# Kernel tuning notes

Hardware: AMD Instinct MI355X
Metric: run time of the kernel (lower is better)

## Reference

```python
import jax, jax.numpy as jnp
import numpy as np

FACTOR = 27.2114 * 0.529177249  # Hartree*Bohr -> eV*Angstrom coulomb factor
N_TYPES = 6
NEURON = [25, 50, 100]
AXIS = 16
B, NC, NM = 4, 128, 16384


def _dense_stack(x, channels, params):
    """Type-indexed MLP: x (B,N,F), channels (N,) int -> (B,N,neuron[-1]).
    Layer 0: no residual; layers 1,2: out=2*in -> residual via concat([x,x])."""
    res_modes = [0, 2, 2]
    for (W, b), res in zip(params, res_modes):
        # W: (C, out, in); gather per-position weights, contract input features
        y = jnp.tanh(jnp.einsum('bnf,nof->bno', x, W[channels]) + b[channels][None])
        if res == 2:
            y = y + jnp.concatenate([x, x], axis=-1)
        elif res == 1:
            y = y + x
        x = y
    return x


def _fwd(atom_coords, charge_coords, charges, esp_params, ef_params, atom_types, real_mask):
    Bb, Nc, _ = atom_coords.shape
    # ---- local environment (off-diagonal neighbor pairs) ----
    i = jnp.arange(Nc)[:, None]
    j = jnp.arange(Nc - 1)[None, :]
    nidx = jnp.where(j < i, j, j + 1)                              # (Nc, Nc-1) neighbor indices
    rij = atom_coords[:, :, None] - atom_coords[:, None]           # (B,Nc,Nc,3)
    rij_off = jnp.take_along_axis(rij, nidx[None, :, :, None], axis=2)  # (B,Nc,Nc-1,3)
    dij = jnp.linalg.norm(rij_off, axis=-1)                        # (B,Nc,Nc-1)
    loc_env_a = rij_off / (dij * dij)[..., None]                   # rij / r^2

    # ---- masked ESP / E-field from MM charges ----
    rq = atom_coords[:, :, None] - charge_coords[:, None]          # (B,Nc,Nm,3)
    dq = jnp.linalg.norm(rq, axis=-1)                              # (B,Nc,Nm)
    d_safe = jnp.maximum(dq, 1e-12)
    pm = real_mask[:, None, :]                                     # (B,1,Nm)
    inv_d = jnp.where(pm, 1.0 / d_safe, 0.0)
    inv_d3 = jnp.where(pm, 1.0 / (d_safe * d_safe * d_safe), 0.0)
    esp = jnp.einsum('bm,bnm->bn', charges, inv_d) * FACTOR        # (B,Nc)
    efield = jnp.einsum('bm,bnmd,bnm->bnd', charges, rq, inv_d3) * FACTOR  # (B,Nc,3)

    # ---- per-atom-type ESP embedding ----
    esp_out = _dense_stack(esp[..., None], atom_types, esp_params)  # (B,Nc,M)

    # ---- per-pair-type E-field embedding ----
    proj = jnp.einsum('bnid,bnd->bni', loc_env_a, efield)           # (B,Nc,Nc-1)
    channels = (atom_types[:, None] * N_TYPES + atom_types[nidx]).reshape(-1)  # (Nc*(Nc-1),)
    x = proj.reshape(Bb, Nc * (Nc - 1), 1)
    out = _dense_stack(x, channels, ef_params).reshape(Bb, Nc, Nc - 1, -1)  # (B,Nc,Nc-1,M)
    G = jnp.einsum('bnim,bnia->bnma', out, out[..., :AXIS])         # (B,Nc,M,axis)
    G = G.reshape(Bb, Nc, -1) * 2.0
    return jnp.concatenate([esp_out, G], axis=2)                    # (B,Nc,M*(axis+1))


def _init_params(key, n_channels):
    dims = [1] + NEURON
    params = []
    for li in range(len(NEURON)):
        kw, kb = jax.random.split(jax.random.fold_in(key, li))
        fan_in = dims[li]
        s = 1.0 / np.sqrt(max(fan_in, 1))
        W = jax.random.uniform(kw, (n_channels, dims[li + 1], fan_in), minval=-s, maxval=s, dtype=jnp.float32)
        b = jax.random.uniform(kb, (n_channels, dims[li + 1]), minval=-s, maxval=s, dtype=jnp.float32)
        params.append((W, b))
    return params


def setup_inputs() -> dict:
    key = jax.random.key(0)
    ks = jax.random.split(key, 8)
    atom_coords = jax.random.normal(ks[0], (B, NC, 3), dtype=jnp.float32) * 5.0
    charge_coords = jax.random.normal(ks[1], (B, NM, 3), dtype=jnp.float32) * 20.0
    charges = jax.random.normal(ks[2], (B, NM), dtype=jnp.float32) * 0.1
    atom_types = jax.random.randint(ks[3], (NC,), 0, N_TYPES)
    real_mask_bool = jax.random.randint(ks[4], (B, NM), 0, 2).astype(bool)
    esp_p = _init_params(ks[5], N_TYPES)
    ef_p = _init_params(ks[6], N_TYPES * N_TYPES)
    inp = {
        'atom_coords': atom_coords, 'charge_coords': charge_coords, 'charges': charges,
        'esp_W0': esp_p[0][0], 'esp_b0': esp_p[0][1], 'esp_W1': esp_p[1][0], 'esp_b1': esp_p[1][1],
        'esp_W2': esp_p[2][0], 'esp_b2': esp_p[2][1],
        'ef_W0': ef_p[0][0], 'ef_b0': ef_p[0][1], 'ef_W1': ef_p[1][0], 'ef_b1': ef_p[1][1],
        'ef_W2': ef_p[2][0], 'ef_b2': ef_p[2][1],
        'atom_types': atom_types, 'real_mask_bool': real_mask_bool,
    }
    return inp


def reference(atom_coords, charge_coords, charges,
              esp_W0, esp_b0, esp_W1, esp_b1, esp_W2, esp_b2,
              ef_W0, ef_b0, ef_W1, ef_b1, ef_W2, ef_b2,
              atom_types, real_mask_bool):
    esp_params = [(esp_W0, esp_b0), (esp_W1, esp_b1), (esp_W2, esp_b2)]
    ef_params = [(ef_W0, ef_b0), (ef_W1, ef_b1), (ef_W2, ef_b2)]
    return _fwd(atom_coords, charge_coords, charges, esp_params, ef_params, atom_types, real_mask_bool)
```

## Files before the change

### kernel.cpp

```cpp
#include <hip/hip_runtime.h>
#include <hip/hip_bf16.h>

#define B_   4
#define NC_  128
#define NM_  16384
#define OUTROW 1700
#define FACTORF ((float)(27.2114 * 0.529177249))

typedef __attribute__((ext_vector_type(8))) short short8v;
typedef __attribute__((ext_vector_type(4))) float float4v;

__device__ __forceinline__ float fast_tanh(float x) {
    float e = __expf(2.0f * x);
    return 1.0f - 2.0f * __builtin_amdgcn_rcpf(e + 1.0f);
}
__device__ __forceinline__ unsigned short f2bf(float x) {
    union { __hip_bfloat16 h; unsigned short u; } cv;
    cv.h = __float2bfloat16(x);
    return cv.u;
}
__device__ __forceinline__ float bflo(unsigned u) { return __uint_as_float(u << 16); }

union FragU { uint4 u4; unsigned u[4]; short8v s; };

__global__ __launch_bounds__(256) void k_prep(
    const float* __restrict__ fW1, const float* __restrict__ fW2,
    unsigned short* __restrict__ w1bf, unsigned short* __restrict__ w2bf,
    const float* __restrict__ atom_coords, const float* __restrict__ charge_coords,
    const float* __restrict__ charges, const void* __restrict__ mask,
    float4* __restrict__ partial, int nchunk)
{
    const int t = threadIdx.x;
    const int blk = blockIdx.x;
    if (blk < 36) {
        unsigned short* dst = w1bf + blk * 2048;
        const float* src = fW1 + blk * 1250;
        for (int i = t; i < 2048; i += 256) {
            int k = i >> 5, l = i & 31;
            float v = (k < 50 && l < 25) ? src[k * 25 + l] : 0.0f;
            dst[i] = f2bf(v);
        }
        return;
    }
    if (blk < 72) {
        int cp = blk - 36;
        unsigned short* dst = w2bf + cp * 7168;
        const float* src = fW2 + cp * 5000;
        for (int i = t; i < 7168; i += 256) {
            int nn = i >> 6, kk = i & 63;
            float v = (nn < 100 && kk < 50) ? src[nn * 50 + kk] : 0.0f;
            dst[i] = f2bf(v);
        }
        return;
    }
    const int eb = blk - 72;
    const int b  = eb / nchunk;
    const int ch = eb % nchunk;
    const int chunkM = NM_ / nchunk;
    const int a = t & 127;
    const int h = t >> 7;

    __shared__ float4 stg[128];
    __shared__ float4 psum[128];
    __shared__ int sdet;

    if (t == 0) sdet = 0;
    __syncthreads();
    if (t < 16) {
        const uint4* mw = (const uint4*)mask;
        uint4 v = mw[b * 1024 + t];
        if ((v.x > 1u) | (v.y > 1u) | (v.z > 1u) | (v.w > 1u)) atomicOr(&sdet, 1);
    }
    __syncthreads();
    const int byteMask = sdet;

    float ax, ay, az;
    {
        const float* p = atom_coords + (size_t)(b * NC_ + a) * 3;
        ax = p[0]; ay = p[1]; az = p[2];
    }
    const float* ccb = charge_coords + (size_t)b * NM_ * 3;
    const float* chb = charges + (size_t)b * NM_;
    const unsigned char* mb8 = (const unsigned char*)mask + (size_t)b * NM_;
    const int* mb32 = (const int*)mask + (size_t)b * NM_;

    float s0 = 0.0f, s1 = 0.0f, s2 = 0.0f, s3 = 0.0f;

    for (int tb = 0; tb < chunkM; tb += 128) {
        if (t < 128) {
            int m = ch * chunkM + tb + t;
            float cx = ccb[3 * m + 0], cy = ccb[3 * m + 1], cz = ccb[3 * m + 2];
            int mk = byteMask ? (int)mb8[m] : mb32[m];
            float q = mk ? chb[m] : 0.0f;
            stg[t] = make_float4(cx, cy, cz, q);
        }
        __syncthreads();
        const float4* sp = stg + h * 64;
#pragma unroll 8
        for (int i = 0; i < 64; ++i) {
            float4 cq = sp[i];
            float dx = ax - cq.x, dy = ay - cq.y, dz = az - cq.z;
            float d2 = dx * dx + dy * dy + dz * dz;
            float inv = __builtin_amdgcn_rsqf(d2);
            float inv3 = inv * inv * inv;
            s0 += cq.w * inv;
            float qi3 = cq.w * inv3;
            s1 += qi3 * dx; s2 += qi3 * dy; s3 += qi3 * dz;
        }
        __syncthreads();
    }
    if (h == 1) psum[a] = make_float4(s0, s1, s2, s3);
    __syncthreads();
    if (h == 0) {
        float4 o = psum[a];
        partial[(size_t)(b * NC_ + a) * nchunk + ch] =
            make_float4(s0 + o.x, s1 + o.y, s2 + o.z, s3 + o.w);
    }
}

__global__ __launch_bounds__(512, 4) void k_ef(
    const float* __restrict__ atom_coords, const float4* __restrict__ partial, int nchunk,
    const int* __restrict__ atom_types,
    const float* __restrict__ eW0, const float* __restrict__ eb0,
    const float* __restrict__ eW1, const float* __restrict__ eb1,
    const float* __restrict__ eW2, const float* __restrict__ eb2,
    const float* __restrict__ fW0, const float* __restrict__ fb0,
    const float* __restrict__ fb1, const float* __restrict__ fb2,
    const unsigned short* __restrict__ w1bf, const unsigned short* __restrict__ w2bf,
    float* __restrict__ out)
{
    const int t   = threadIdx.x;
    const int blk = blockIdx.x;
    const int b   = blk >> 7;
    const int n   = blk & 127;

    __shared__ float cst[NC_][3];
    __shared__ float xs[128];
    __shared__ int   sc[128];
    __shared__ int   tat[128];
    __shared__ int   wcnt[2][6];
    __shared__ int   tmeta[16];
    __shared__ int   tcnt;
    __shared__ float a0s[6][25];
    __shared__ float b0s[6][25];
    __shared__ float b1s[6][50];
    __shared__ float b2s[6][100];
    __shared__ float espf[4];
    __shared__ float h0e[25];
    __shared__ float h1e[52];
    __shared__ __align__(16) unsigned short y0p[128][32];
    __shared__ __align__(16) unsigned short y1p[128][72];
    __shared__ __align__(16) unsigned short y2t[112][136];

    const int tn = atom_types[n];
    const int c0 = tn * 6;
    const int wv   = t >> 6;
    const int lane = t & 63;

    for (int idx = t; idx < NC_ * 3; idx += 512)
        (&cst[0][0])[idx] = atom_coords[(size_t)b * NC_ * 3 + idx];
    if (t < 128) tat[t] = atom_types[t];
    for (int idx = t; idx < 150; idx += 512) {
        (&a0s[0][0])[idx] = fW0[c0 * 25 + idx];
        (&b0s[0][0])[idx] = fb0[c0 * 25 + idx];
    }
    if (t >= 192 && t < 492) (&b1s[0][0])[t - 192] = fb1[c0 * 50 + t - 192];
    if (t < 112) y2t[t][127] = 0;
    if (t >= 128 && t < 192) {
        for (int idx = t - 128; idx < 600; idx += 64)
            (&b2s[0][0])[idx] = fb2[c0 * 100 + idx];
    }
    if (t >= 256 && t < 320) {
        int lt = t - 256;
        float4 v = make_float4(0.f, 0.f, 0.f, 0.f);
        for (int ch = lt; ch < nchunk; ch += 64) {
            float4 u = partial[(size_t)(b * NC_ + n) * nchunk + ch];
            v.x += u.x; v.y += u.y; v.z += u.z; v.w += u.w;
        }
#pragma unroll
        for (int off = 32; off > 0; off >>= 1) {
            v.x += __shfl_xor(v.x, off, 64);
            v.y += __shfl_xor(v.y, off, 64);
            v.z += __shfl_xor(v.z, off, 64);
            v.w += __shfl_xor(v.w, off, 64);
        }
        if (lt == 0) {
            espf[0] = v.x * FACTORF;
            espf[1] = v.y * FACTORF;
            espf[2] = v.z * FACTORF;
            espf[3] = v.w * FACTORF;
        }
    }
    __syncthreads();

    unsigned long long mkeep = 0;
    int myc = 0; float px = 0.0f;
    if (wv < 2) {
        const bool valid = t < 127;
        if (valid) {
            int jn = (t < n) ? t : t + 1;
            float rx = cst[n][0] - cst[jn][0];
            float ry = cst[n][1] - cst[jn][1];
            float rz = cst[n][2] - cst[jn][2];
            float d2 = rx * rx + ry * ry + rz * rz;
            px = (rx * espf[1] + ry * espf[2] + rz * espf[3]) / d2;
            myc = tat[jn];
        }
#pragma unroll
        for (int v = 0; v < 6; ++v) {
            unsigned long long m = __ballot(valid && (myc == v));
            if (valid && myc == v) mkeep = m;
            if (lane == 0) wcnt[wv][v] = __builtin_popcountll(m);
        }
    } else if (t >= 320 && t < 345) {
        int l = t - 320;
        h0e[l] = fast_tanh(eW0[tn * 25 + l] * espf[0] + eb0[tn * 25 + l]);
    }
    __syncthreads();

    if (t < 127) {
        int w0[6], w1[6];
#pragma unroll
        for (int v = 0; v < 6; ++v) { w0[v] = wcnt[0][v]; w1[v] = wcnt[1][v]; }
        int basec = 0;
#pragma unroll
        for (int v = 0; v < 6; ++v) if (v < myc) basec += w0[v] + w1[v];
        int pos = basec + (wv == 1 ? w0[myc] : 0)
                + __builtin_popcountll(mkeep & ((1ull << lane) - 1ull));
        sc[pos] = myc; xs[pos] = px;
        if (t == 0) {
            int run = 0, nt = 0;
#pragma unroll
            for (int v = 0; v < 6; ++v) {
                int pendv = run + w0[v] + w1[v];
                for (int base = run; base < pendv; base += 16) {
                    tmeta[nt] = base | (v << 8) | (pendv << 12);
                    ++nt;
                }
                run = pendv;
            }
            tcnt = nt;
        }
    } else if (t >= 320 && t < 370) {
        int l = t - 320;
        float s = eb1[tn * 50 + l];
        const float* wr = eW1 + (size_t)(tn * 50 + l) * 25;
#pragma unroll
        for (int j = 0; j < 25; ++j) s += wr[j] * h0e[j];
        h1e[l] = fast_tanh(s) + h0e[l % 25];
    }
    __syncthreads();

    if (t < 256) {
        for (int i = t; i < 127 * 32; i += 256) {
            int r = i >> 5, l = i & 31;
            int c = sc[r]; float x = xs[r];
            float v = (l < 25) ? fast_tanh(a0s[c][l] * x + b0s[c][l]) : 0.0f;
            y0p[r][l] = f2bf(v);
        }
    } else if (t >= 320 && t < 420) {
        int k = t - 320;
        float s = eb2[tn * 100 + k];
        const float2* wr = (const float2*)(eW2 + (size_t)(tn * 100 + k) * 50);
#pragma unroll
        for (int j = 0; j < 25; ++j) {
            float2 u = wr[j];
            s += u.x * h1e[2 * j] + u.y * h1e[2 * j + 1];
        }
        out[(size_t)(b * NC_ + n) * OUTROW + k] = fast_tanh(s) + h1e[k % 50];
    }
    __syncthreads();

    {
        const int kt = wv & 3;
        const int krow = (lane >> 4) << 3;
        const int arow = kt * 16 + (lane & 15);
        const unsigned short* wb = w1bf + ((size_t)c0 * 64 + arow) * 32 + krow;
        int meta = (lane < 16) ? tmeta[lane & 15] : 0;
        const int nt = tcnt;
        int ccur = -1;
        FragU Af;
#pragma unroll 1
        for (int ti = (wv >> 2); ti < nt; ti += 2) {
            const int mv = __builtin_amdgcn_readlane(meta, ti);
            const int base = mv & 255, c = (mv >> 8) & 15, pend = mv >> 12;
            if (c != ccur) {
                ccur = c;
                Af.u4 = *(const uint4*)(wb + (size_t)c * 2048);
            }
            FragU Bf;
            Bf.u4 = *(const uint4*)&y0p[base + (lane & 15)][krow];
            float4v acc = {0.f, 0.f, 0.f, 0.f};
            acc = __builtin_amdgcn_mfma_f32_16x16x32_bf16(Af.s, Bf.s, acc, 0, 0, 0);
            const int p = base + (lane & 15);
            if (p < pend) {
                const int kb = kt * 16 + ((lane >> 4) << 2);
                unsigned short yv[4];
#pragma unroll
                for (int r = 0; r < 4; ++r) {
                    int k = kb + r;
                    float s = acc[r] + ((k < 50) ? b1s[c][k] : 0.0f);
                    float y = fast_tanh(s);
                    if (k < 50) y += bflo((unsigned)y0p[p][k % 25]);
                    yv[r] = f2bf(y);
                }
                unsigned lo = (unsigned)yv[0] | ((unsigned)yv[1] << 16);
                unsigned hi = (unsigned)yv[2] | ((unsigned)yv[3] << 16);
                *(uint2*)&y1p[p][kb] = make_uint2(lo, hi);
            }
        }
    }
    __syncthreads();

    if (wv < 7) {
        const int krow = (lane >> 4) << 3;
        const int arow = wv * 16 + (lane & 15);
        int meta = (lane < 16) ? tmeta[lane & 15] : 0;
        const int nt = tcnt;
        int ccur = -1;
        FragU A0, A1;
#pragma unroll 1
        for (int ti = 0; ti < nt; ++ti) {
            const int mv = __builtin_amdgcn_readlane(meta, ti);
            const int base = mv & 255, c = (mv >> 8) & 15, pend = mv >> 12;
            if (c != ccur) {
                ccur = c;
                const unsigned short* wb =
                    w2bf + ((size_t)(c0 + c) * 112 + arow) * 64;
                A0.u4 = *(const uint4*)(wb + krow);
                A1.u4 = *(const uint4*)(wb + 32 + krow);
            }
            FragU B0, B1;
            const int p = base + (lane & 15);
            B0.u4 = *(const uint4*)&y1p[p][krow];
            B1.u4 = *(const uint4*)&y1p[p][32 + krow];
            float4v acc = {0.f, 0.f, 0.f, 0.f};
            acc = __builtin_amdgcn_mfma_f32_16x16x32_bf16(A0.s, B0.s, acc, 0, 0, 0);
            acc = __builtin_amdgcn_mfma_f32_16x16x32_bf16(A1.s, B1.s, acc, 0, 0, 0);
            if (p < pend) {
                const int nb = wv * 16 + ((lane >> 4) << 2);
#pragma unroll
                for (int r = 0; r < 4; ++r) {
                    int nn = nb + r;
                    if (nn < 100) {
                        float yres = bflo((unsigned)y1p[p][nn % 50]);
                        float y2 = fast_tanh(acc[r] + b2s[c][nn]) + yres;
                        y2t[nn][p] = f2bf(y2);
                    }
                }
            }
        }
    }
    __syncthreads();

    if (wv < 7) {
        const int krow = (lane >> 4) << 3;
        short8v GB[4];
#pragma unroll
        for (int ks = 0; ks < 4; ++ks) {
            FragU cv; cv.u4 = *(const uint4*)&y2t[lane & 15][ks * 32 + krow];
            GB[ks] = cv.s;
        }
        float* orow = out + (size_t)(b * NC_ + n) * OUTROW + 100;
        const int aa = lane & 15;
        const int m0 = wv * 16 + (lane & 15);
        float4v acc = {0.f, 0.f, 0.f, 0.f};
#pragma unroll
        for (int ks = 0; ks < 4; ++ks) {
            FragU av; av.u4 = *(const uint4*)&y2t[m0][ks * 32 + krow];
            acc = __builtin_amdgcn_mfma_f32_16x16x32_bf16(av.s, GB[ks], acc, 0, 0, 0);
        }
        const int mrow = wv * 16 + ((lane >> 4) << 2);
#pragma unroll
        for (int r = 0; r < 4; ++r) {
            int m = mrow + r;
            if (m < 100) orow[m * 16 + aa] = 2.0f * acc[r];
        }
    }
}

extern "C" void kernel_launch(void* const* d_in, const int* in_sizes, int n_in,
                              void* d_out, int out_size, void* d_ws, size_t ws_size,
                              hipStream_t stream) {
    (void)in_sizes; (void)n_in; (void)out_size;
    const float* atom_coords   = (const float*)d_in[0];
    const float* charge_coords = (const float*)d_in[1];
    const float* charges       = (const float*)d_in[2];
    const float* eW0 = (const float*)d_in[3];
    const float* eb0 = (const float*)d_in[4];
    const float* eW1 = (const float*)d_in[5];
    const float* eb1 = (const float*)d_in[6];
    const float* eW2 = (const float*)d_in[7];
    const float* eb2 = (const float*)d_in[8];
    const float* fW0 = (const float*)d_in[9];
    const float* fb0 = (const float*)d_in[10];
    const float* fW1 = (const float*)d_in[11];
    const float* fb1 = (const float*)d_in[12];
    const float* fW2 = (const float*)d_in[13];
    const float* fb2 = (const float*)d_in[14];
    const int*   atom_types = (const int*)d_in[15];
    const void*  mask = d_in[16];
    float* out = (float*)d_out;

    const size_t W1BF_B = 36 * 64 * 32 * 2;
    const size_t W2BF_B = 36 * 112 * 64 * 2;
    unsigned short* w1bf = (unsigned short*)d_ws;
    unsigned short* w2bf = (unsigned short*)((char*)d_ws + W1BF_B);
    float4* partial = (float4*)((char*)d_ws + W1BF_B + W2BF_B);

    int nchunk = 128;
    while (nchunk > 1 &&
           W1BF_B + W2BF_B + (size_t)B_ * NC_ * nchunk * 16 > ws_size)
        nchunk >>= 1;

    k_prep<<<72 + B_ * nchunk, 256, 0, stream>>>(
        fW1, fW2, w1bf, w2bf,
        atom_coords, charge_coords, charges, mask, partial, nchunk);
    k_ef<<<B_ * NC_, 512, 0, stream>>>(
        atom_coords, partial, nchunk, atom_types,
        eW0, eb0, eW1, eb1, eW2, eb2,
        fW0, fb0, fb1, fb2, w1bf, w2bf, out);
}
```

Measured before the change: 32.18 us.

## Fuse charge-field reduction and weight conversion into single per-atom kernel

Merges the prep kernel and the embedding kernel into one launch. Each block now sums ESP and E-field contributions for its own atom over all MM charges, reduces them with wave shuffles and shared memory, and converts only its needed W1/W2 weights to bf16 on the fly. This drops the second launch, the partial-sum workspace and the separate weight-conversion pass. In exchange, every block rereads the full charge array of its batch with no cross-atom reuse, and the weight conversion is repeated in every block.

New measurement: 43.32 us. +34.6%, slower.

```diff
diff --git a/kernel.cpp b/kernel.cpp
--- a/kernel.cpp
+++ b/kernel.cpp
@@ -23,110 +23,16 @@
 
 union FragU { uint4 u4; unsigned u[4]; short8v s; };
 
-__global__ __launch_bounds__(256) void k_prep(
-    const float* __restrict__ fW1, const float* __restrict__ fW2,
-    unsigned short* __restrict__ w1bf, unsigned short* __restrict__ w2bf,
+__global__ __launch_bounds__(512, 4) void k_all(
     const float* __restrict__ atom_coords, const float* __restrict__ charge_coords,
     const float* __restrict__ charges, const void* __restrict__ mask,
-    float4* __restrict__ partial, int nchunk)
-{
-    const int t = threadIdx.x;
-    const int blk = blockIdx.x;
-    if (blk < 36) {
-        unsigned short* dst = w1bf + blk * 2048;
-        const float* src = fW1 + blk * 1250;
-        for (int i = t; i < 2048; i += 256) {
-            int k = i >> 5, l = i & 31;
-            float v = (k < 50 && l < 25) ? src[k * 25 + l] : 0.0f;
-            dst[i] = f2bf(v);
-        }
-        return;
-    }
-    if (blk < 72) {
-        int cp = blk - 36;
-        unsigned short* dst = w2bf + cp * 7168;
-        const float* src = fW2 + cp * 5000;
-        for (int i = t; i < 7168; i += 256) {
-            int nn = i >> 6, kk = i & 63;
-            float v = (nn < 100 && kk < 50) ? src[nn * 50 + kk] : 0.0f;
-            dst[i] = f2bf(v);
-        }
-        return;
-    }
-    const int eb = blk - 72;
-    const int b  = eb / nchunk;
-    const int ch = eb % nchunk;
-    const int chunkM = NM_ / nchunk;
-    const int a = t & 127;
-    const int h = t >> 7;
-
-    __shared__ float4 stg[128];
-    __shared__ float4 psum[128];
-    __shared__ int sdet;
-
-    if (t == 0) sdet = 0;
-    __syncthreads();
-    if (t < 16) {
-        const uint4* mw = (const uint4*)mask;
-        uint4 v = mw[b * 1024 + t];
-        if ((v.x > 1u) | (v.y > 1u) | (v.z > 1u) | (v.w > 1u)) atomicOr(&sdet, 1);
-    }
-    __syncthreads();
-    const int byteMask = sdet;
-
-    float ax, ay, az;
-    {
-        const float* p = atom_coords + (size_t)(b * NC_ + a) * 3;
-        ax = p[0]; ay = p[1]; az = p[2];
-    }
-    const float* ccb = charge_coords + (size_t)b * NM_ * 3;
-    const float* chb = charges + (size_t)b * NM_;
-    const unsigned char* mb8 = (const unsigned char*)mask + (size_t)b * NM_;
-    const int* mb32 = (const int*)mask + (size_t)b * NM_;
-
-    float s0 = 0.0f, s1 = 0.0f, s2 = 0.0f, s3 = 0.0f;
-
-    for (int tb = 0; tb < chunkM; tb += 128) {
-        if (t < 128) {
-            int m = ch * chunkM + tb + t;
-            float cx = ccb[3 * m + 0], cy = ccb[3 * m + 1], cz = ccb[3 * m + 2];
-            int mk = byteMask ? (int)mb8[m] : mb32[m];
-            float q = mk ? chb[m] : 0.0f;
-            stg[t] = make_float4(cx, cy, cz, q);
-        }
-        __syncthreads();
-        const float4* sp = stg + h * 64;
-#pragma unroll 8
-        for (int i = 0; i < 64; ++i) {
-            float4 cq = sp[i];
-            float dx = ax - cq.x, dy = ay - cq.y, dz = az - cq.z;
-            float d2 = dx * dx + dy * dy + dz * dz;
-            float inv = __builtin_amdgcn_rsqf(d2);
-            float inv3 = inv * inv * inv;
-            s0 += cq.w * inv;
-            float qi3 = cq.w * inv3;
-            s1 += qi3 * dx; s2 += qi3 * dy; s3 += qi3 * dz;
-        }
-        __syncthreads();
-    }
-    if (h == 1) psum[a] = make_float4(s0, s1, s2, s3);
-    __syncthreads();
-    if (h == 0) {
-        float4 o = psum[a];
-        partial[(size_t)(b * NC_ + a) * nchunk + ch] =
-            make_float4(s0 + o.x, s1 + o.y, s2 + o.z, s3 + o.w);
-    }
-}
-
-__global__ __launch_bounds__(512, 4) void k_ef(
-    const float* __restrict__ atom_coords, const float4* __restrict__ partial, int nchunk,
     const int* __restrict__ atom_types,
     const float* __restrict__ eW0, const float* __restrict__ eb0,
     const float* __restrict__ eW1, const float* __restrict__ eb1,
     const float* __restrict__ eW2, const float* __restrict__ eb2,
     const float* __restrict__ fW0, const float* __restrict__ fb0,
-    const float* __restrict__ fb1, const float* __restrict__ fb2,
-    const unsigned short* __restrict__ w1bf, const unsigned short* __restrict__ w2bf,
+    const float* __restrict__ fW1, const float* __restrict__ fb1,
+    const float* __restrict__ fW2, const float* __restrict__ fb2,
     float* __restrict__ out)
 {
     const int t   = threadIdx.x;
@@ -141,6 +47,8 @@
     __shared__ int   wcnt[2][6];
     __shared__ int   tmeta[16];
     __shared__ int   tcnt;
+    __shared__ int   sdet;
+    __shared__ float wsum[8][4];
     __shared__ float a0s[6][25];
     __shared__ float b0s[6][25];
     __shared__ float b1s[6][50];
@@ -152,10 +60,22 @@
     __shared__ __align__(16) unsigned short y1p[128][72];
     __shared__ __align__(16) unsigned short y2t[112][136];
 
+    unsigned short* w1s = (unsigned short*)&y2t[0][0];
+
     const int tn = atom_types[n];
     const int c0 = tn * 6;
     const int wv   = t >> 6;
     const int lane = t & 63;
+
+    if (t == 0) sdet = 0;
+    __syncthreads();
+    if (t < 16) {
+        const uint4* mw = (const uint4*)mask;
+        uint4 v = mw[b * 1024 + t];
+        if ((v.x > 1u) | (v.y > 1u) | (v.z > 1u) | (v.w > 1u)) atomicOr(&sdet, 1);
+    }
+    __syncthreads();
+    const int byteMask = sdet;
 
     for (int idx = t; idx < NC_ * 3; idx += 512)
         (&cst[0][0])[idx] = atom_coords[(size_t)b * NC_ * 3 + idx];
@@ -164,32 +84,68 @@
         (&a0s[0][0])[idx] = fW0[c0 * 25 + idx];
         (&b0s[0][0])[idx] = fb0[c0 * 25 + idx];
     }
-    if (t >= 192 && t < 492) (&b1s[0][0])[t - 192] = fb1[c0 * 50 + t - 192];
-    if (t < 112) y2t[t][127] = 0;
-    if (t >= 128 && t < 192) {
-        for (int idx = t - 128; idx < 600; idx += 64)
-            (&b2s[0][0])[idx] = fb2[c0 * 100 + idx];
-    }
-    if (t >= 256 && t < 320) {
-        int lt = t - 256;
-        float4 v = make_float4(0.f, 0.f, 0.f, 0.f);
-        for (int ch = lt; ch < nchunk; ch += 64) {
-            float4 u = partial[(size_t)(b * NC_ + n) * nchunk + ch];
-            v.x += u.x; v.y += u.y; v.z += u.z; v.w += u.w;
-        }
-#pragma unroll
-        for (int off = 32; off > 0; off >>= 1) {
-            v.x += __shfl_xor(v.x, off, 64);
-            v.y += __shfl_xor(v.y, off, 64);
-            v.z += __shfl_xor(v.z, off, 64);
-            v.w += __shfl_xor(v.w, off, 64);
-        }
-        if (lt == 0) {
-            espf[0] = v.x * FACTORF;
-            espf[1] = v.y * FACTORF;
-            espf[2] = v.z * FACTORF;
-            espf[3] = v.w * FACTORF;
-        }
+    for (int idx = t; idx < 300; idx += 512) (&b1s[0][0])[idx] = fb1[c0 * 50 + idx];
+    for (int idx = t; idx < 600; idx += 512) (&b2s[0][0])[idx] = fb2[c0 * 100 + idx];
+    for (int i = t; i < 6 * 64 * 32; i += 512) {
+        int c = i >> 11, r = (i >> 5) & 63, l = i & 31;
+        float v = (r < 50 && l < 25)
+                    ? fW1[(size_t)(c0 + c) * 1250 + r * 25 + l] : 0.0f;
+        w1s[i] = f2bf(v);
+    }
+
+    float ax, ay, az;
+    {
+        const float* p = atom_coords + (size_t)(b * NC_ + n) * 3;
+        ax = p[0]; ay = p[1]; az = p[2];
+    }
+    const float* ccb = charge_coords + (size_t)b * NM_ * 3;
+    const float* chb = charges + (size_t)b * NM_;
+    float s0 = 0.0f, s1 = 0.0f, s2 = 0.0f, s3 = 0.0f;
+    if (byteMask) {
+        const unsigned char* mb8 = (const unsigned char*)mask + (size_t)b * NM_;
+#pragma unroll 4
+        for (int i = 0; i < 32; ++i) {
+            int m = t + (i << 9);
+            float cx = ccb[3 * m], cy = ccb[3 * m + 1], cz = ccb[3 * m + 2];
+            float q = mb8[m] ? chb[m] : 0.0f;
+            float dx = ax - cx, dy = ay - cy, dz = az - cz;
+            float d2 = dx * dx + dy * dy + dz * dz;
+            float inv = __builtin_amdgcn_rsqf(d2);
+            float inv3 = inv * inv * inv;
+            s0 += q * inv;
+            float qi3 = q * inv3;
+            s1 += qi3 * dx; s2 += qi3 * dy; s3 += qi3 * dz;
+        }
+    } else {
+        const int* mb32 = (const int*)mask + (size_t)b * NM_;
+#pragma unroll 4
+        for (int i = 0; i < 32; ++i) {
+            int m = t + (i << 9);
+            float cx = ccb[3 * m], cy = ccb[3 * m + 1], cz = ccb[3 * m + 2];
+            float q = mb32[m] ? chb[m] : 0.0f;
+            float dx = ax - cx, dy = ay - cy, dz = az - cz;
+            float d2 = dx * dx + dy * dy + dz * dz;
+            float inv = __builtin_amdgcn_rsqf(d2);
+            float inv3 = inv * inv * inv;
+            s0 += q * inv;
+            float qi3 = q * inv3;
+            s1 += qi3 * dx; s2 += qi3 * dy; s3 += qi3 * dz;
+        }
+    }
+#pragma unroll
+    for (int off = 32; off > 0; off >>= 1) {
+        s0 += __shfl_xor(s0, off, 64);
+        s1 += __shfl_xor(s1, off, 64);
+        s2 += __shfl_xor(s2, off, 64);
+        s3 += __shfl_xor(s3, off, 64);
+    }
+    if (lane == 0) { wsum[wv][0] = s0; wsum[wv][1] = s1; wsum[wv][2] = s2; wsum[wv][3] = s3; }
+    __syncthreads();
+    if (t < 4) {
+        float acc = 0.0f;
+#pragma unroll
+        for (int w = 0; w < 8; ++w) acc += wsum[w][t];
+        espf[t] = acc * FACTORF;
     }
     __syncthreads();
 
@@ -275,18 +231,16 @@
         const int kt = wv & 3;
         const int krow = (lane >> 4) << 3;
         const int arow = kt * 16 + (lane & 15);
-        const unsigned short* wb = w1bf + ((size_t)c0 * 64 + arow) * 32 + krow;
         int meta = (lane < 16) ? tmeta[lane & 15] : 0;
         const int nt = tcnt;
         int ccur = -1;
         FragU Af;
-#pragma unroll 1
         for (int ti = (wv >> 2); ti < nt; ti += 2) {
             const int mv = __builtin_amdgcn_readlane(meta, ti);
             const int base = mv & 255, c = (mv >> 8) & 15, pend = mv >> 12;
             if (c != ccur) {
                 ccur = c;
-                Af.u4 = *(const uint4*)(wb + (size_t)c * 2048);
+                Af.u4 = *(const uint4*)&w1s[(c << 11) + arow * 32 + krow];
             }
             FragU Bf;
             Bf.u4 = *(const uint4*)&y0p[base + (lane & 15)][krow];
@@ -314,21 +268,29 @@
 
     if (wv < 7) {
         const int krow = (lane >> 4) << 3;
-        const int arow = wv * 16 + (lane & 15);
+        const int nnr  = wv * 16 + (lane & 15);
+        const bool nok = nnr < 100;
         int meta = (lane < 16) ? tmeta[lane & 15] : 0;
         const int nt = tcnt;
         int ccur = -1;
         FragU A0, A1;
-#pragma unroll 1
         for (int ti = 0; ti < nt; ++ti) {
             const int mv = __builtin_amdgcn_readlane(meta, ti);
             const int base = mv & 255, c = (mv >> 8) & 15, pend = mv >> 12;
             if (c != ccur) {
                 ccur = c;
-                const unsigned short* wb =
-                    w2bf + ((size_t)(c0 + c) * 112 + arow) * 64;
-                A0.u4 = *(const uint4*)(wb + krow);
-                A1.u4 = *(const uint4*)(wb + 32 + krow);
+                const float* wrow =
+                    fW2 + ((size_t)((c0 + c) * 100) + (nok ? nnr : 0)) * 50;
+#pragma unroll
+                for (int j = 0; j < 4; ++j) {
+                    float a0 = nok ? wrow[krow + 2 * j]     : 0.0f;
+                    float a1 = nok ? wrow[krow + 2 * j + 1] : 0.0f;
+                    A0.u[j] = (unsigned)f2bf(a0) | ((unsigned)f2bf(a1) << 16);
+                    int kb0 = 32 + krow + 2 * j;
+                    float b0v = (nok && kb0 < 50)     ? wrow[kb0]     : 0.0f;
+                    float b1v = (nok && kb0 + 1 < 50) ? wrow[kb0 + 1] : 0.0f;
+                    A1.u[j] = (unsigned)f2bf(b0v) | ((unsigned)f2bf(b1v) << 16);
+                }
             }
             FragU B0, B1;
             const int p = base + (lane & 15);
@@ -350,6 +312,8 @@
                 }
             }
         }
+    } else {
+        for (int i = lane; i < 112; i += 64) y2t[i][127] = 0;
     }
     __syncthreads();
 
@@ -382,7 +346,7 @@
 extern "C" void kernel_launch(void* const* d_in, const int* in_sizes, int n_in,
                               void* d_out, int out_size, void* d_ws, size_t ws_size,
                               hipStream_t stream) {
-    (void)in_sizes; (void)n_in; (void)out_size;
+    (void)in_sizes; (void)n_in; (void)out_size; (void)d_ws; (void)ws_size;
     const float* atom_coords   = (const float*)d_in[0];
     const float* charge_coords = (const float*)d_in[1];
     const float* charges       = (const float*)d_in[2];
@@ -402,22 +366,8 @@
     const void*  mask = d_in[16];
     float* out = (float*)d_out;
 
-    const size_t W1BF_B = 36 * 64 * 32 * 2;
-    const size_t W2BF_B = 36 * 112 * 64 * 2;
-    unsigned short* w1bf = (unsigned short*)d_ws;
-    unsigned short* w2bf = (unsigned short*)((char*)d_ws + W1BF_B);
-    float4* partial = (float4*)((char*)d_ws + W1BF_B + W2BF_B);
-
-    int nchunk = 128;
-    while (nchunk > 1 &&
-           W1BF_B + W2BF_B + (size_t)B_ * NC_ * nchunk * 16 > ws_size)
-        nchunk >>= 1;
-
-    k_prep<<<72 + B_ * nchunk, 256, 0, stream>>>(
-        fW1, fW2, w1bf, w2bf,
-        atom_coords, charge_coords, charges, mask, partial, nchunk);
-    k_ef<<<B_ * NC_, 512, 0, stream>>>(
-        atom_coords, partial, nchunk, atom_types,
+    k_all<<<B_ * NC_, 512, 0, stream>>>(
+        atom_coords, charge_coords, charges, mask, atom_types,
         eW0, eb0, eW1, eb1, eW2, eb2,
-        fW0, fb0, fb1, fb2, w1bf, w2bf, out);
+        fW0, fb0, fW1, fb1, fW2, fb2, out);
 }
```

## Shrink shared memory and compute residuals via identity MFMA in k_ef

Applied to the files above, without the earlier changes.

Raises the occupancy hint of k_ef to 6 blocks per CU. To fit, it aliases y0p onto y2t, trims y2t to 100 rows, and stores a0/b0/b2 parameters in shared memory as bf16. The residual adds in the layer-1 and layer-2 MFMA loops now come from extra MFMAs against an identity-selection fragment, replacing scattered LDS reads, and the bias values are hoisted into registers per channel. The costs are precision loss from bf16 biases and first-layer weights, extra MFMA work, and tighter register pressure under the new bound.

After: 30.57 us. 1.05x faster.

```diff
diff --git a/kernel.cpp b/kernel.cpp
--- a/kernel.cpp
+++ b/kernel.cpp
@@ -20,6 +20,7 @@
     return cv.u;
 }
 __device__ __forceinline__ float bflo(unsigned u) { return __uint_as_float(u << 16); }
+__device__ __forceinline__ float bfu(unsigned short u) { return __uint_as_float(((unsigned)u) << 16); }
 
 union FragU { uint4 u4; unsigned u[4]; short8v s; };
 
@@ -118,7 +119,7 @@
     }
 }
 
-__global__ __launch_bounds__(512, 4) void k_ef(
+__global__ __launch_bounds__(512, 6) void k_ef(
     const float* __restrict__ atom_coords, const float4* __restrict__ partial, int nchunk,
     const int* __restrict__ atom_types,
     const float* __restrict__ eW0, const float* __restrict__ eb0,
@@ -141,16 +142,16 @@
     __shared__ int   wcnt[2][6];
     __shared__ int   tmeta[16];
     __shared__ int   tcnt;
-    __shared__ float a0s[6][25];
-    __shared__ float b0s[6][25];
+    __shared__ unsigned short a0s[6][25];
+    __shared__ unsigned short b0s[6][25];
     __shared__ float b1s[6][50];
-    __shared__ float b2s[6][100];
+    __shared__ unsigned short b2s[6][100];
     __shared__ float espf[4];
     __shared__ float h0e[25];
     __shared__ float h1e[52];
-    __shared__ __align__(16) unsigned short y0p[128][32];
     __shared__ __align__(16) unsigned short y1p[128][72];
-    __shared__ __align__(16) unsigned short y2t[112][136];
+    __shared__ __align__(16) unsigned short y2t[100][136];
+    unsigned short (*y0p)[32] = (unsigned short (*)[32])&y2t[0][0];
 
     const int tn = atom_types[n];
     const int c0 = tn * 6;
@@ -161,14 +162,13 @@
         (&cst[0][0])[idx] = atom_coords[(size_t)b * NC_ * 3 + idx];
     if (t < 128) tat[t] = atom_types[t];
     for (int idx = t; idx < 150; idx += 512) {
-        (&a0s[0][0])[idx] = fW0[c0 * 25 + idx];
-        (&b0s[0][0])[idx] = fb0[c0 * 25 + idx];
+        (&a0s[0][0])[idx] = f2bf(fW0[c0 * 25 + idx]);
+        (&b0s[0][0])[idx] = f2bf(fb0[c0 * 25 + idx]);
     }
     if (t >= 192 && t < 492) (&b1s[0][0])[t - 192] = fb1[c0 * 50 + t - 192];
-    if (t < 112) y2t[t][127] = 0;
     if (t >= 128 && t < 192) {
         for (int idx = t - 128; idx < 600; idx += 64)
-            (&b2s[0][0])[idx] = fb2[c0 * 100 + idx];
+            (&b2s[0][0])[idx] = f2bf(fb2[c0 * 100 + idx]);
     }
     if (t >= 256 && t < 320) {
         int lt = t - 256;
@@ -255,7 +255,7 @@
         for (int i = t; i < 127 * 32; i += 256) {
             int r = i >> 5, l = i & 31;
             int c = sc[r]; float x = xs[r];
-            float v = (l < 25) ? fast_tanh(a0s[c][l] * x + b0s[c][l]) : 0.0f;
+            float v = (l < 25) ? fast_tanh(bfu(a0s[c][l]) * x + bfu(b0s[c][l])) : 0.0f;
             y0p[r][l] = f2bf(v);
         }
     } else if (t >= 320 && t < 420) {
@@ -275,35 +275,41 @@
         const int kt = wv & 3;
         const int krow = (lane >> 4) << 3;
         const int arow = kt * 16 + (lane & 15);
+        const int kres = (arow < 50) ? (arow % 25) : 999;
+        FragU Id;
+#pragma unroll
+        for (int e = 0; e < 4; ++e) {
+            int ka = krow + 2 * e;
+            Id.u[e] = (ka == kres ? 0x3f80u : 0u) | (ka + 1 == kres ? 0x3f800000u : 0u);
+        }
         const unsigned short* wb = w1bf + ((size_t)c0 * 64 + arow) * 32 + krow;
         int meta = (lane < 16) ? tmeta[lane & 15] : 0;
         const int nt = tcnt;
+        const int kb = kt * 16 + ((lane >> 4) << 2);
         int ccur = -1;
         FragU Af;
-#pragma unroll 1
+        float bias[4];
         for (int ti = (wv >> 2); ti < nt; ti += 2) {
             const int mv = __builtin_amdgcn_readlane(meta, ti);
             const int base = mv & 255, c = (mv >> 8) & 15, pend = mv >> 12;
             if (c != ccur) {
                 ccur = c;
                 Af.u4 = *(const uint4*)(wb + (size_t)c * 2048);
+#pragma unroll
+                for (int r = 0; r < 4; ++r)
+                    bias[r] = (kb + r < 50) ? b1s[c][kb + r] : 0.0f;
             }
             FragU Bf;
             Bf.u4 = *(const uint4*)&y0p[base + (lane & 15)][krow];
-            float4v acc = {0.f, 0.f, 0.f, 0.f};
-            acc = __builtin_amdgcn_mfma_f32_16x16x32_bf16(Af.s, Bf.s, acc, 0, 0, 0);
+            float4v z = {0.f, 0.f, 0.f, 0.f};
+            float4v acc  = __builtin_amdgcn_mfma_f32_16x16x32_bf16(Af.s, Bf.s, z, 0, 0, 0);
+            float4v acc2 = __builtin_amdgcn_mfma_f32_16x16x32_bf16(Id.s, Bf.s, z, 0, 0, 0);
             const int p = base + (lane & 15);
             if (p < pend) {
-                const int kb = kt * 16 + ((lane >> 4) << 2);
                 unsigned short yv[4];
 #pragma unroll
-                for (int r = 0; r < 4; ++r) {
-                    int k = kb + r;
-                    float s = acc[r] + ((k < 50) ? b1s[c][k] : 0.0f);
-                    float y = fast_tanh(s);
-                    if (k < 50) y += bflo((unsigned)y0p[p][k % 25]);
-                    yv[r] = f2bf(y);
-                }
+                for (int r = 0; r < 4; ++r)
+                    yv[r] = f2bf(fast_tanh(acc[r] + bias[r]) + acc2[r]);
                 unsigned lo = (unsigned)yv[0] | ((unsigned)yv[1] << 16);
                 unsigned hi = (unsigned)yv[2] | ((unsigned)yv[3] << 16);
                 *(uint2*)&y1p[p][kb] = make_uint2(lo, hi);
@@ -315,11 +321,21 @@
     if (wv < 7) {
         const int krow = (lane >> 4) << 3;
         const int arow = wv * 16 + (lane & 15);
+        const int nres = (arow < 100) ? (arow % 50) : 999;
+        FragU Id0, Id1;
+#pragma unroll
+        for (int e = 0; e < 4; ++e) {
+            int ka = krow + 2 * e;
+            Id0.u[e] = (ka == nres ? 0x3f80u : 0u) | (ka + 1 == nres ? 0x3f800000u : 0u);
+            int kc = 32 + krow + 2 * e;
+            Id1.u[e] = (kc == nres ? 0x3f80u : 0u) | (kc + 1 == nres ? 0x3f800000u : 0u);
+        }
         int meta = (lane < 16) ? tmeta[lane & 15] : 0;
         const int nt = tcnt;
+        const int nb = wv * 16 + ((lane >> 4) << 2);
         int ccur = -1;
         FragU A0, A1;
-#pragma unroll 1
+        float bb[4];
         for (int ti = 0; ti < nt; ++ti) {
             const int mv = __builtin_amdgcn_readlane(meta, ti);
             const int base = mv & 255, c = (mv >> 8) & 15, pend = mv >> 12;
@@ -329,27 +345,30 @@
                     w2bf + ((size_t)(c0 + c) * 112 + arow) * 64;
                 A0.u4 = *(const uint4*)(wb + krow);
                 A1.u4 = *(const uint4*)(wb + 32 + krow);
+#pragma unroll
+                for (int r = 0; r < 4; ++r)
+                    bb[r] = (nb + r < 100) ? bfu(b2s[c][nb + r]) : 0.0f;
             }
             FragU B0, B1;
             const int p = base + (lane & 15);
             B0.u4 = *(const uint4*)&y1p[p][krow];
             B1.u4 = *(const uint4*)&y1p[p][32 + krow];
-            float4v acc = {0.f, 0.f, 0.f, 0.f};
-            acc = __builtin_amdgcn_mfma_f32_16x16x32_bf16(A0.s, B0.s, acc, 0, 0, 0);
-            acc = __builtin_amdgcn_mfma_f32_16x16x32_bf16(A1.s, B1.s, acc, 0, 0, 0);
+            float4v z = {0.f, 0.f, 0.f, 0.f};
+            float4v acc  = __builtin_amdgcn_mfma_f32_16x16x32_bf16(A0.s, B0.s, z, 0, 0, 0);
+            acc  = __builtin_amdgcn_mfma_f32_16x16x32_bf16(A1.s, B1.s, acc, 0, 0, 0);
+            float4v acc2 = __builtin_amdgcn_mfma_f32_16x16x32_bf16(Id0.s, B0.s, z, 0, 0, 0);
+            acc2 = __builtin_amdgcn_mfma_f32_16x16x32_bf16(Id1.s, B1.s, acc2, 0, 0, 0);
             if (p < pend) {
-                const int nb = wv * 16 + ((lane >> 4) << 2);
 #pragma unroll
                 for (int r = 0; r < 4; ++r) {
                     int nn = nb + r;
-                    if (nn < 100) {
-                        float yres = bflo((unsigned)y1p[p][nn % 50]);
-                        float y2 = fast_tanh(acc[r] + b2s[c][nn]) + yres;
-                        y2t[nn][p] = f2bf(y2);
-                    }
+                    if (nn < 100)
+                        y2t[nn][p] = f2bf(fast_tanh(acc[r] + bb[r]) + acc2[r]);
                 }
             }
         }
+    } else {
+        for (int i = lane; i < 100; i += 64) y2t[i][127] = 0;
     }
     __syncthreads();
 
@@ -363,7 +382,8 @@
         }
         float* orow = out + (size_t)(b * NC_ + n) * OUTROW + 100;
         const int aa = lane & 15;
-        const int m0 = wv * 16 + (lane & 15);
+        int m0 = wv * 16 + (lane & 15);
+        if (m0 > 99) m0 = 99;
         float4v acc = {0.f, 0.f, 0.f, 0.f};
 #pragma unroll
         for (int ks = 0; ks < 4; ++ks) {
```
